# Kernel tuning notes

Measured on AMD Instinct MI355X. Metric: run time of the kernel, lower is better.

The kernel has to match this reference:

```python
import jax, jax.numpy as jnp
import numpy as np

N = 100000   # nodes
E = 1600000  # edges
IN_DIM = 64
OUT_DIM = 64
HEADS = 4
C = OUT_DIM // HEADS  # per-head channels = 16
EDGE_DIM = 16
NEG_SLOPE = 0.2
EPS = 1e-5


def setup_inputs() -> dict:
    key = jax.random.key(0)
    ks = jax.random.split(key, 16)
    s = 0.1
    return {
        "x": jax.random.normal(ks[0], (N, IN_DIM), jnp.float32),
        "edge_index": jax.random.randint(ks[1], (2, E), 0, N, jnp.int64 if jax.config.jax_enable_x64 else jnp.int32),
        "edge_attr": jax.random.normal(ks[2], (E, EDGE_DIM), jnp.float32),
        # GATv2Conv params (share_weights=False, edge_dim, concat=True)
        "Wl": jax.random.normal(ks[3], (IN_DIM, HEADS * C), jnp.float32) * s,
        "bl": jnp.zeros((HEADS * C,), jnp.float32),
        "Wr": jax.random.normal(ks[4], (IN_DIM, HEADS * C), jnp.float32) * s,
        "br": jnp.zeros((HEADS * C,), jnp.float32),
        "We": jax.random.normal(ks[5], (EDGE_DIM, HEADS * C), jnp.float32) * s,
        "att": jax.random.normal(ks[6], (HEADS, C), jnp.float32) * s,
        "conv_bias": jnp.zeros((HEADS * C,), jnp.float32),
        # edge gate MLP: Linear(edge_dim, 2*edge_dim) -> SiLU -> Linear(2*edge_dim, 1) -> Sigmoid
        "Wg1": jax.random.normal(ks[7], (EDGE_DIM, 2 * EDGE_DIM), jnp.float32) * s,
        "bg1": jnp.zeros((2 * EDGE_DIM,), jnp.float32),
        "Wg2": jax.random.normal(ks[8], (2 * EDGE_DIM, 1), jnp.float32) * s,
        "bg2": jnp.zeros((1,), jnp.float32),
        # LayerNorm(out_dim)
        "gamma": jnp.ones((OUT_DIM,), jnp.float32),
        "beta": jnp.zeros((OUT_DIM,), jnp.float32),
    }


def _silu(v):
    return v * jax.nn.sigmoid(v)


def reference(x, edge_index, edge_attr, Wl, bl, Wr, br, We, att, conv_bias,
              Wg1, bg1, Wg2, bg2, gamma, beta):
    src, tgt = edge_index[0], edge_index[1]

    # --- edge gate: sigmoid(Linear(SiLU(Linear(e)))) -> [E, 1]
    gate = jax.nn.sigmoid(_silu(edge_attr @ Wg1 + bg1) @ Wg2 + bg2)

    # --- GATv2Conv ---
    xl = (x @ Wl + bl).reshape(N, HEADS, C)   # source transform
    xr = (x @ Wr + br).reshape(N, HEADS, C)   # target transform
    ee = (edge_attr @ We).reshape(E, HEADS, C)

    xj = xl[src]                               # [E, H, C] source messages
    m = jax.nn.leaky_relu(xj + xr[tgt] + ee, NEG_SLOPE)
    alpha = jnp.einsum('ehc,hc->eh', m, att)   # [E, H]

    # segment softmax over edges sharing the same target node
    amax = jax.ops.segment_max(alpha, tgt, num_segments=N)  # [N, H]
    a = jnp.exp(alpha - amax[tgt])
    denom = jax.ops.segment_sum(a, tgt, num_segments=N)
    a = a / denom[tgt]

    out = jax.ops.segment_sum(xj * a[:, :, None], tgt, num_segments=N)
    out = out.reshape(N, HEADS * C) + conv_bias

    # --- edge-gate mean modulation per target node ---
    gate_sum = jax.ops.segment_sum(gate[:, 0], tgt, num_segments=N)
    degree = jax.ops.segment_sum(jnp.ones((E,), out.dtype), tgt, num_segments=N)
    mean_gate = gate_sum / jnp.maximum(degree, 1.0)
    out = out * mean_gate[:, None]

    # --- LayerNorm -> SiLU -> (dropout p=0) -> residual (Identity proj) ---
    mu = jnp.mean(out, axis=-1, keepdims=True)
    var = jnp.var(out, axis=-1, keepdims=True)
    out = (out - mu) * jax.lax.rsqrt(var + EPS) * gamma + beta
    out = _silu(out)
    return out + x
```

## Files before the change

kernel.cpp:

```cpp
#include <hip/hip_runtime.h>
#include <hip/hip_bf16.h>
#include <hip/hip_fp16.h>
#include <math.h>

#define N_NODES 100000
#define N_EDGES 1600000
#define IN_DIM 64
#define OUT_DIM 64
#define HEADS 4
#define CH 16
#define EDGE_DIM 16
#define NEG_SLOPE 0.2f
#define LN_EPS 1e-5f
#define NBLK 391
#define CHUNK 32
#define NREP 8
#define WS_NEED_EAH 127203168ull

typedef unsigned short u16;
typedef unsigned int u32;
typedef unsigned long long u64;
typedef __attribute__((ext_vector_type(8))) short bf16x8;
typedef __attribute__((ext_vector_type(4))) float f32x4;
typedef __attribute__((ext_vector_type(2))) _Float16 f16x2;

__device__ __forceinline__ float bf2f(u16 v) {
    return __uint_as_float(((u32)v) << 16);
}
__device__ __forceinline__ u16 f2bf(float f) {
    u32 u = __float_as_uint(f);
    u32 r = (u + 0x7FFFu + ((u >> 16) & 1u)) >> 16;
    return (u16)r;
}
__device__ __forceinline__ float fdot2f(u32 a, u32 b, float c) {
    return __builtin_amdgcn_fdot2(__builtin_bit_cast(f16x2, a),
                                  __builtin_bit_cast(f16x2, b), c, false);
}
__device__ __forceinline__ u32 packf16(float lo, float hi) {
    f16x2 p;
    p[0] = (_Float16)lo;
    p[1] = (_Float16)hi;
    return __builtin_bit_cast(u32, p);
}
__device__ __forceinline__ void load16bf(const u16* p, float* out) {
    const uint4* q = (const uint4*)p;
    uint4 a = q[0], b = q[1];
    u32 w[8] = {a.x, a.y, a.z, a.w, b.x, b.y, b.z, b.w};
#pragma unroll
    for (int i = 0; i < 8; ++i) {
        out[2*i]   = __uint_as_float(w[i] << 16);
        out[2*i+1] = __uint_as_float(w[i] & 0xFFFF0000u);
    }
}
__device__ __forceinline__ void load16f(const void* base, long i, bool f32in, float* out) {
    if (f32in) {
        const float4* q = (const float4*)((const float*)base + i);
        float4 v0 = q[0], v1 = q[1], v2 = q[2], v3 = q[3];
        out[0]=v0.x; out[1]=v0.y; out[2]=v0.z; out[3]=v0.w;
        out[4]=v1.x; out[5]=v1.y; out[6]=v1.z; out[7]=v1.w;
        out[8]=v2.x; out[9]=v2.y; out[10]=v2.z; out[11]=v2.w;
        out[12]=v3.x; out[13]=v3.y; out[14]=v3.z; out[15]=v3.w;
    } else {
        load16bf((const u16*)base + i, out);
    }
}
__device__ __forceinline__ float ldf(const void* base, int i, bool f32in) {
    return f32in ? ((const float*)base)[i] : bf2f(((const u16*)base)[i]);
}

#define DPP_ROR_ADD(v, N) do { \
    int _d = __builtin_amdgcn_update_dpp(0, __float_as_int(v), 0x120 + (N), 0xF, 0xF, true); \
    (v) += __int_as_float(_d); } while (0)

__global__ void k_sniff_zero(const u32* __restrict__ xw, const int* __restrict__ eiw,
                             int* __restrict__ flags, int4* __restrict__ curR4,
                             float4* __restrict__ gsum4) {
    if (blockIdx.x != 0) {
        const int i = (blockIdx.x - 1) * 256 + threadIdx.x;
        if (i < NREP * N_NODES / 4) curR4[i] = make_int4(0, 0, 0, 0);
        else if (i < NREP * N_NODES / 4 + N_NODES / 4)
            gsum4[i - NREP * N_NODES / 4] = make_float4(0.f, 0.f, 0.f, 0.f);
        return;
    }
    __shared__ int s_f32, s_not64;
    const int t = threadIdx.x;
    if (t == 0) { s_f32 = 0; s_not64 = 0; }
    __syncthreads();
    if (t < 64) {
        u32 w = xw[t];
        for (int h = 0; h < 2; ++h) {
            u32 bits = h ? (w & 0xFFFF0000u) : (w << 16);
            float v = __uint_as_float(bits);
            float a = fabsf(v);
            bool sane = (a == 0.0f) || (a >= 1e-30f && a <= 1000.0f);
            if (!sane || v != v) atomicOr(&s_f32, 1);
        }
    } else if (t < 96) {
        if (eiw[2 * (t - 64) + 1] != 0) atomicOr(&s_not64, 1);
    }
    __syncthreads();
    if (t == 0) flags[0] = s_f32 | ((s_not64 ? 0 : 1) << 1);
}

__global__ __launch_bounds__(256) void k_transform(
    const void* __restrict__ x,
    const void* __restrict__ Wl, const void* __restrict__ bl,
    const void* __restrict__ Wr, const void* __restrict__ br,
    u16* __restrict__ xl, u16* __restrict__ xr,
    const int* __restrict__ flags)
{
    const bool f32in = (flags[0] & 1) != 0;
    const int lane = threadIdx.x & 63;
    const int w = threadIdx.x >> 6;
    const int m0 = blockIdx.x * 64;
    const int col = lane & 15;
    const int quad = lane >> 4;

    bf16x8 bfrag[2][2];
    float bias[2];
#pragma unroll
    for (int nt = 0; nt < 2; ++nt) {
        const int ng = w * 32 + nt * 16 + col;
        const void* W  = (ng < 64) ? Wl : Wr;
        const void* bi = (ng < 64) ? bl : br;
        const int c = ng & 63;
        bias[nt] = ldf(bi, c, f32in);
#pragma unroll
        for (int kf = 0; kf < 2; ++kf)
#pragma unroll
            for (int j = 0; j < 8; ++j) {
                const int k = kf * 32 + quad * 8 + j;
                bfrag[nt][kf][j] = (short)f2bf(ldf(W, k * 64 + c, f32in));
            }
    }

#pragma unroll
    for (int mt = 0; mt < 4; ++mt) {
        const int mrow = m0 + mt * 16 + col;
        const int m = (mrow < N_NODES) ? mrow : (N_NODES - 1);
        bf16x8 afrag[2];
#pragma unroll
        for (int kf = 0; kf < 2; ++kf) {
            const int kb = kf * 32 + quad * 8;
            if (f32in) {
                const float* xp = (const float*)x + (size_t)m * 64 + kb;
#pragma unroll
                for (int j = 0; j < 8; ++j) afrag[kf][j] = (short)f2bf(xp[j]);
            } else {
                afrag[kf] = *(const bf16x8*)((const u16*)x + (size_t)m * 64 + kb);
            }
        }
#pragma unroll
        for (int nt = 0; nt < 2; ++nt) {
            f32x4 c = {bias[nt], bias[nt], bias[nt], bias[nt]};
            c = __builtin_amdgcn_mfma_f32_16x16x32_bf16(afrag[0], bfrag[nt][0], c, 0, 0, 0);
            c = __builtin_amdgcn_mfma_f32_16x16x32_bf16(afrag[1], bfrag[nt][1], c, 0, 0, 0);
            const int ng = w * 32 + nt * 16 + col;
            u16* dst = (ng < 64) ? xl : xr;
            const int cc = ng & 63;
#pragma unroll
            for (int r = 0; r < 4; ++r) {
                const int node = m0 + mt * 16 + quad * 4 + r;
                if (node < N_NODES) dst[(size_t)node * 64 + cc] = f2bf(c[r]);
            }
        }
    }
}

__global__ __launch_bounds__(256) void k_count_gate(
    const int* __restrict__ ei, int* __restrict__ curR,
    float4* __restrict__ zreg, u16* __restrict__ slotA, u16* __restrict__ gateA,
    u16* __restrict__ eaH, const int write_eah,
    const void* __restrict__ edge_attr,
    const void* __restrict__ Wg1, const void* __restrict__ bg1,
    const void* __restrict__ Wg2, const void* __restrict__ bg2,
    const int* __restrict__ flags)
{
    __shared__ float sWg1t[32 * 16];
    __shared__ float sBg1[32];
    __shared__ float sWg2[32];
    __shared__ float sBg2;
    const int tid = threadIdx.x;
    const int fl = flags[0];
    const bool f32in = (fl & 1) != 0;
    const bool i64   = (fl & 2) != 0;
    for (int i = tid; i < 32 * 16; i += 256) {
        const int j = i >> 4, k = i & 15;
        sWg1t[i] = ldf(Wg1, k * 32 + j, f32in);
    }
    if (tid < 32) sBg1[tid] = ldf(bg1, tid, f32in);
    if (tid >= 32 && tid < 64) sWg2[tid - 32] = ldf(Wg2, tid - 32, f32in);
    if (tid == 0) sBg2 = ldf(bg2, 0, f32in);
    __syncthreads();

    const int gid = blockIdx.x * 256 + tid;
    for (int i = gid; i < N_NODES * 68 / 4; i += 6250 * 256)
        zreg[i] = make_float4(0.f, 0.f, 0.f, 0.f);
    const int tgt = i64 ? ei[2 * (N_EDGES + gid)] : ei[N_EDGES + gid];
    const int r = blockIdx.x & (NREP - 1);
    const int slot = atomicAdd(&curR[r * N_NODES + tgt], 1);
    slotA[gid] = (u16)slot;

    float ea[EDGE_DIM];
    load16f(edge_attr, (long)gid * EDGE_DIM, f32in, ea);

    if (write_eah) {
        u32 h[8];
#pragma unroll
        for (int i = 0; i < 8; ++i) h[i] = packf16(ea[2*i], ea[2*i+1]);
        uint4* dst = (uint4*)(eaH + (size_t)gid * 16);
        dst[0] = make_uint4(h[0], h[1], h[2], h[3]);
        dst[1] = make_uint4(h[4], h[5], h[6], h[7]);
    }

    float g = sBg2;
#pragma unroll
    for (int j = 0; j < 32; ++j) {
        float hv = sBg1[j];
        const float4* wr = (const float4*)&sWg1t[j * 16];
#pragma unroll
        for (int k4 = 0; k4 < 4; ++k4) {
            const float4 wv = wr[k4];
            hv += ea[4*k4]   * wv.x + ea[4*k4+1] * wv.y
                + ea[4*k4+2] * wv.z + ea[4*k4+3] * wv.w;
        }
        hv = hv / (1.f + __expf(-hv));
        g += hv * sWg2[j];
    }
    g = 1.f / (1.f + __expf(-g));
    gateA[gid] = __half_as_ushort(__float2half(g));
}

__global__ __launch_bounds__(256) void k_bsum(const int* __restrict__ curR,
                                              int* __restrict__ partial)
{
    const int i = blockIdx.x * 256 + threadIdx.x;
    int v = 0;
    if (i < N_NODES) {
#pragma unroll
        for (int r = 0; r < NREP; ++r) v += curR[r * N_NODES + i];
    }
#pragma unroll
    for (int off = 32; off >= 1; off >>= 1) v += __shfl_xor(v, off, 64);
    __shared__ int ws[4];
    if ((threadIdx.x & 63) == 0) ws[threadIdx.x >> 6] = v;
    __syncthreads();
    if (threadIdx.x == 0) partial[blockIdx.x] = ws[0] + ws[1] + ws[2] + ws[3];
}

__global__ void k_bscan(const int* __restrict__ partial, int* __restrict__ poff,
                        int* __restrict__ base)
{
    __shared__ int sp[NBLK];
    for (int i = threadIdx.x; i < NBLK; i += 64) sp[i] = partial[i];
    __syncthreads();
    if (threadIdx.x == 0) {
        int run = 0;
        for (int i = 0; i < NBLK; ++i) { int t = sp[i]; sp[i] = run; run += t; }
        base[N_NODES] = N_EDGES;
    }
    __syncthreads();
    for (int i = threadIdx.x; i < NBLK; i += 64) poff[i] = sp[i];
}

__global__ __launch_bounds__(256) void k_bfinal(int* __restrict__ curR,
                                                const int* __restrict__ poff,
                                                int* __restrict__ base)
{
    const int i = blockIdx.x * 256 + threadIdx.x;
    const int lane = threadIdx.x & 63;
    const int wave = threadIdx.x >> 6;
    int c[NREP];
    int v = 0;
    if (i < N_NODES) {
#pragma unroll
        for (int r = 0; r < NREP; ++r) { c[r] = curR[r * N_NODES + i]; v += c[r]; }
    }
    int s = v;
#pragma unroll
    for (int off = 1; off < 64; off <<= 1) {
        int t = __shfl_up(s, off, 64);
        if (lane >= off) s += t;
    }
    __shared__ int wsum[4];
    if (lane == 63) wsum[wave] = s;
    __syncthreads();
    int wb = 0;
    for (int w = 0; w < wave; ++w) wb += wsum[w];
    if (i < N_NODES) {
        int run = poff[blockIdx.x] + wb + s - v;
        base[i] = run;
#pragma unroll
        for (int r = 0; r < NREP; ++r) { curR[r * N_NODES + i] = run; run += c[r]; }
    }
}

__global__ __launch_bounds__(256) void k_scatter(
    const int* __restrict__ ei, const int* __restrict__ curR,
    const u16* __restrict__ slotA,
    u64* __restrict__ perm8, const int* __restrict__ flags)
{
    const int e = blockIdx.x * 256 + threadIdx.x;
    const bool i64 = (flags[0] & 2) != 0;
    int src, tgt;
    if (i64) { src = ei[2 * e]; tgt = ei[2 * (N_EDGES + e)]; }
    else     { src = ei[e];     tgt = ei[N_EDGES + e]; }
    const int r = blockIdx.x & (NREP - 1);
    const int pos = curR[r * N_NODES + tgt] + (int)slotA[e];
    perm8[pos] = (u64)(u32)src | ((u64)(u32)tgt << 17) | ((u64)(u32)e << 34);
}


__device__ __forceinline__ void seg_flush(
    float* __restrict__ accum, float* __restrict__ dsum_g, float* __restrict__ gsum,
    int t, int lane, float acc, float dsum, float gs)
{
    atomicAdd(&accum[(size_t)t * 64 + lane], acc);
    if ((lane & 15) == 0) atomicAdd(&dsum_g[t * 4 + (lane >> 4)], dsum);
    if (lane == 1) atomicAdd(&gsum[t], gs);
}

template<bool F32IN, bool EAH>
__device__ __forceinline__ void ea_fetch(const void* __restrict__ edge_attr,
                                         const u16* __restrict__ eaH,
                                         int eid, uint4* r)
{
    if constexpr (EAH) {
        const uint4* q = (const uint4*)(eaH + (size_t)eid * 16);
        r[0] = q[0]; r[1] = q[1];
    } else if constexpr (F32IN) {
        const uint4* q = (const uint4*)edge_attr + (size_t)eid * 4;
        r[0] = q[0]; r[1] = q[1]; r[2] = q[2]; r[3] = q[3];
    } else {
        const uint4* q = (const uint4*)((const u16*)edge_attr + (size_t)eid * 16);
        r[0] = q[0]; r[1] = q[1];
    }
}

template<bool F32IN>
__device__ __forceinline__ void ea_vals(const uint4* r, float* out)
{
    const u32* w = (const u32*)r;
    if constexpr (F32IN) {
#pragma unroll
        for (int i = 0; i < 16; ++i) out[i] = __uint_as_float(w[i]);
    } else {
#pragma unroll
        for (int i = 0; i < 8; ++i) {
            out[2*i]   = __uint_as_float(w[i] << 16);
            out[2*i+1] = __uint_as_float(w[i] & 0xFFFF0000u);
        }
    }
}

#define PERM_EXTRACT(JJ, S, T, E2) do { \
    const u32 _lo = (u32)__builtin_amdgcn_readlane(plo, (JJ)); \
    const u32 _hi = (u32)__builtin_amdgcn_readlane(phi, (JJ)); \
    (S)  = (int)(_lo & 0x1FFFFu); \
    (T)  = (int)(((_lo >> 17) | (_hi << 15)) & 0x1FFFFu); \
    (E2) = (int)(_hi >> 2); } while (0)

template<bool F32IN, bool EAH>
__device__ __forceinline__ void attn_run(
    const u64* __restrict__ perm8, const void* __restrict__ edge_attr,
    const u16* __restrict__ eaH, const u16* __restrict__ gateA,
    const u16* __restrict__ xl, const u16* __restrict__ xr,
    float* __restrict__ accum, float* __restrict__ dsum_g, float* __restrict__ gsum,
    const float* We_c, const u32* We2, float att_c, int lane, int j0)
{
    const u64 pl = perm8[j0 + (lane & (CHUNK - 1))];
    const int plo = (int)(u32)pl;
    const int phi = (int)(u32)(pl >> 32);

    int s_cur, t_cur, e_cur;
    PERM_EXTRACT(0, s_cur, t_cur, e_cur);

    constexpr int NU4 = EAH ? 2 : (F32IN ? 4 : 2);
    uint4 eb[2][NU4];
    ea_fetch<F32IN, EAH>(edge_attr, eaH, e_cur, eb[0]);
    u32 xl_c = xl[(size_t)s_cur * 64 + lane];
    u32 xr_c = xr[(size_t)t_cur * 64 + lane];
    float g_c = __half2float(__ushort_as_half(gateA[e_cur]));

    int cur_t = t_cur;
    float acc = 0.f, dsum = 0.f, gs = 0.f;

#pragma unroll
    for (int jj = 0; jj < CHUNK; ++jj) {
        const int cb = jj & 1;
        int s_nxt = s_cur, t_nxt = t_cur, e_nxt = e_cur;
        u32 xl_n = xl_c, xr_n = xr_c;
        float g_n = g_c;
        if (jj + 1 < CHUNK) {
            PERM_EXTRACT(jj + 1, s_nxt, t_nxt, e_nxt);
            ea_fetch<F32IN, EAH>(edge_attr, eaH, e_nxt, eb[cb ^ 1]);
            xl_n = xl[(size_t)s_nxt * 64 + lane];
            g_n = __half2float(__ushort_as_half(gateA[e_nxt]));
            if (t_nxt != t_cur)
                xr_n = xr[(size_t)t_nxt * 64 + lane];
        }

        const float xlf = bf2f((u16)xl_c);
        const float xrf = bf2f((u16)xr_c);

        if (t_cur != cur_t) {
            seg_flush(accum, dsum_g, gsum, cur_t, lane, acc, dsum, gs);
            cur_t = t_cur; acc = 0.f; dsum = 0.f; gs = 0.f;
        }

        float m = xlf + xrf;
        if constexpr (EAH) {
            const u32* w = (const u32*)eb[cb];
#pragma unroll
            for (int i = 0; i < 8; ++i) m = fdot2f(w[i], We2[i], m);
        } else {
            float eav[16];
            ea_vals<F32IN>(eb[cb], eav);
#pragma unroll
            for (int k = 0; k < EDGE_DIM; ++k) m = fmaf(eav[k], We_c[k], m);
        }
        m = fmaxf(m, m * NEG_SLOPE);
        float t = att_c * m;
        DPP_ROR_ADD(t, 1);
        DPP_ROR_ADD(t, 2);
        DPP_ROR_ADD(t, 4);
        DPP_ROR_ADD(t, 8);
        const float a = __expf(t);
        acc  += a * xlf;
        dsum += a;
        gs   += g_c;

        s_cur = s_nxt; t_cur = t_nxt; e_cur = e_nxt;
        xl_c = xl_n;   xr_c = xr_n;   g_c = g_n;
    }
    seg_flush(accum, dsum_g, gsum, cur_t, lane, acc, dsum, gs);
}

template<bool EAH>
__global__ __launch_bounds__(256, 8) void k_attn_agg(
    const u64* __restrict__ perm8,
    const void* __restrict__ edge_attr,
    const u16* __restrict__ eaH,
    const u16* __restrict__ gateA,
    const void* __restrict__ We,
    const void* __restrict__ att,
    const u16* __restrict__ xl, const u16* __restrict__ xr,
    float* __restrict__ accum,
    float* __restrict__ dsum_g,
    float* __restrict__ gsum,
    const int* __restrict__ flags)
{
    const bool f32in = (flags[0] & 1) != 0;
    const int lane = threadIdx.x & 63;
    const int wid = blockIdx.x * 4 + (threadIdx.x >> 6);
    const int j0 = wid * CHUNK;

    float We_c[EDGE_DIM];
#pragma unroll
    for (int k = 0; k < EDGE_DIM; ++k) We_c[k] = ldf(We, k * 64 + lane, f32in);
    u32 We2[8];
    if constexpr (EAH) {
#pragma unroll
        for (int i = 0; i < 8; ++i) We2[i] = packf16(We_c[2*i], We_c[2*i+1]);
    }
    const float att_c = ldf(att, lane, f32in);

    if (f32in) attn_run<true , EAH>(perm8, edge_attr, eaH, gateA, xl, xr,
                                    accum, dsum_g, gsum, We_c, We2, att_c, lane, j0);
    else       attn_run<false, EAH>(perm8, edge_attr, eaH, gateA, xl, xr,
                                    accum, dsum_g, gsum, We_c, We2, att_c, lane, j0);
}

__global__ __launch_bounds__(256) void k_epilogue(
    const int* __restrict__ base,
    const float* __restrict__ accum, const float* __restrict__ dsum_g,
    const float* __restrict__ gsum,
    const void* __restrict__ conv_bias, const void* __restrict__ gamma,
    const void* __restrict__ beta, const void* __restrict__ x,
    void* __restrict__ out, const int* __restrict__ flags)
{
    const bool f32in = (flags[0] & 1) != 0;
    const int lane = threadIdx.x & 63;
    const int wave = threadIdx.x >> 6;
    const int n = blockIdx.x * 4 + wave;
    if (n >= N_NODES) return;
    const int h = lane >> 4;

    float v = accum[(size_t)n * 64 + lane];
    const float d = dsum_g[n * 4 + h];
    v = (d > 0.f) ? v / d : 0.f;
    v += ldf(conv_bias, lane, f32in);
    const int deg = base[n + 1] - base[n];
    const float mg = gsum[n] / fmaxf((float)deg, 1.0f);
    v *= mg;

    float s = v;
#pragma unroll
    for (int m2 = 32; m2 >= 1; m2 >>= 1) s += __shfl_xor(s, m2, 64);
    const float mu = s * (1.f / 64.f);
    const float diff = v - mu;
    float q = diff * diff;
#pragma unroll
    for (int m2 = 32; m2 >= 1; m2 >>= 1) q += __shfl_xor(q, m2, 64);
    const float var = q * (1.f / 64.f);

    float y = diff * rsqrtf(var + LN_EPS) * ldf(gamma, lane, f32in) + ldf(beta, lane, f32in);
    y = y / (1.f + __expf(-y));
    const float r = y + ldf(x, n * 64 + lane, f32in);
    if (f32in) ((float*)out)[(size_t)n * 64 + lane] = r;
    else       ((u16*)out)[(size_t)n * 64 + lane] = f2bf(r);
}

extern "C" void kernel_launch(void* const* d_in, const int* in_sizes, int n_in,
                              void* d_out, int out_size, void* d_ws, size_t ws_size,
                              hipStream_t stream)
{
    const void* x   = d_in[0];
    const int* ei   = (const int*)d_in[1];
    const void* ea  = d_in[2];
    const void* Wl  = d_in[3];
    const void* bl  = d_in[4];
    const void* Wr  = d_in[5];
    const void* br  = d_in[6];
    const void* We  = d_in[7];
    const void* att = d_in[8];
    const void* cb  = d_in[9];
    const void* Wg1 = d_in[10];
    const void* bg1 = d_in[11];
    const void* Wg2 = d_in[12];
    const void* bg2 = d_in[13];
    const void* gam = d_in[14];
    const void* bet = d_in[15];

    char* ws = (char*)d_ws;
    int*   flags   = (int*)ws;
    int*   curR    = (int*)(ws + 16);
    int*   base    = (int*)(ws + 3200016);
    int*   partial = (int*)(ws + 3600032);
    int*   poff    = (int*)(ws + 3601600);
    u16*   slotA   = (u16*)(ws + 3603168);
    u16*   gateA   = (u16*)(ws + 6803168);
    u64*   perm8   = (u64*)(ws + 10003168);
    float* accum   = (float*)(ws + 22803168);
    float* dsum_g  = (float*)(ws + 48403168);
    float* gsum    = (float*)(ws + 50003168);
    u16*   xl      = (u16*)(ws + 50403168);
    u16*   xr      = (u16*)(ws + 63203168);
    u16*   eaH     = (u16*)(ws + 76003168);

    const int eah = (ws_size >= WS_NEED_EAH) ? 1 : 0;

    k_sniff_zero<<<881, 256, 0, stream>>>((const u32*)x, ei, flags, (int4*)curR,
                                          (float4*)gsum);

    k_transform<<<(N_NODES + 63) / 64, 256, 0, stream>>>(x, Wl, bl, Wr, br, xl, xr, flags);

    k_count_gate<<<N_EDGES / 256, 256, 0, stream>>>(
        ei, curR, (float4*)accum, slotA, gateA, eaH, eah, ea, Wg1, bg1, Wg2, bg2, flags);

    k_bsum<<<NBLK, 256, 0, stream>>>(curR, partial);
    k_bscan<<<1, 64, 0, stream>>>(partial, poff, base);
    k_bfinal<<<NBLK, 256, 0, stream>>>(curR, poff, base);

    k_scatter<<<N_EDGES / 256, 256, 0, stream>>>(ei, curR, slotA, perm8, flags);

    if (eah)
        k_attn_agg<true ><<<N_EDGES / CHUNK / 4, 256, 0, stream>>>(
            perm8, ea, eaH, gateA, We, att, xl, xr, accum, dsum_g, gsum, flags);
    else
        k_attn_agg<false><<<N_EDGES / CHUNK / 4, 256, 0, stream>>>(
            perm8, ea, eaH, gateA, We, att, xl, xr, accum, dsum_g, gsum, flags);

    k_epilogue<<<(N_NODES + 3) / 4, 256, 0, stream>>>(
        base, accum, dsum_g, gsum, cb, gam, bet, x, d_out, flags);
}
```

Measured before the change: 476.7 us.

## Permute fp16 edge attributes and pack gate into perm during scatter

Moves the fp16 conversion of edge attributes from the gate kernel into the scatter kernel. The scatter now writes them in target-sorted order, so the attention kernel reads them sequentially instead of gathering by edge id. The fp16 gate value is packed into the perm entry in place of the edge id, which removes the random gateA gather. The cost is that the scatter writes are now random 32-byte stores and the scatter kernel re-reads edge_attr.

```diff
diff --git a/kernel.cpp b/kernel.cpp
--- a/kernel.cpp
+++ b/kernel.cpp
@@ -15,7 +15,7 @@
 #define NBLK 391
 #define CHUNK 32
 #define NREP 8
-#define WS_NEED_EAH 127203168ull
+#define WS_NEED_STREAM 127203168ull
 
 typedef unsigned short u16;
 typedef unsigned int u32;
@@ -170,7 +170,6 @@
 __global__ __launch_bounds__(256) void k_count_gate(
     const int* __restrict__ ei, int* __restrict__ curR,
     float4* __restrict__ zreg, u16* __restrict__ slotA, u16* __restrict__ gateA,
-    u16* __restrict__ eaH, const int write_eah,
     const void* __restrict__ edge_attr,
     const void* __restrict__ Wg1, const void* __restrict__ bg1,
     const void* __restrict__ Wg2, const void* __restrict__ bg2,
@@ -204,15 +203,6 @@
     float ea[EDGE_DIM];
     load16f(edge_attr, (long)gid * EDGE_DIM, f32in, ea);
 
-    if (write_eah) {
-        u32 h[8];
-#pragma unroll
-        for (int i = 0; i < 8; ++i) h[i] = packf16(ea[2*i], ea[2*i+1]);
-        uint4* dst = (uint4*)(eaH + (size_t)gid * 16);
-        dst[0] = make_uint4(h[0], h[1], h[2], h[3]);
-        dst[1] = make_uint4(h[4], h[5], h[6], h[7]);
-    }
-
     float g = sBg2;
 #pragma unroll
     for (int j = 0; j < 32; ++j) {
@@ -297,17 +287,35 @@
 
 __global__ __launch_bounds__(256) void k_scatter(
     const int* __restrict__ ei, const int* __restrict__ curR,
-    const u16* __restrict__ slotA,
+    const u16* __restrict__ slotA, const u16* __restrict__ gateA,
+    const void* __restrict__ edge_attr, u16* __restrict__ eaP,
+    const int stream_mode,
     u64* __restrict__ perm8, const int* __restrict__ flags)
 {
     const int e = blockIdx.x * 256 + threadIdx.x;
-    const bool i64 = (flags[0] & 2) != 0;
+    const int fl = flags[0];
+    const bool f32in = (fl & 1) != 0;
+    const bool i64   = (fl & 2) != 0;
     int src, tgt;
     if (i64) { src = ei[2 * e]; tgt = ei[2 * (N_EDGES + e)]; }
     else     { src = ei[e];     tgt = ei[N_EDGES + e]; }
     const int r = blockIdx.x & (NREP - 1);
     const int pos = curR[r * N_NODES + tgt] + (int)slotA[e];
-    perm8[pos] = (u64)(u32)src | ((u64)(u32)tgt << 17) | ((u64)(u32)e << 34);
+
+    if (stream_mode) {
+        const u32 gate = gateA[e];
+        perm8[pos] = (u64)(u32)src | ((u64)(u32)tgt << 17) | ((u64)gate << 34);
+        float ea[EDGE_DIM];
+        load16f(edge_attr, (long)e * EDGE_DIM, f32in, ea);
+        u32 h[8];
+#pragma unroll
+        for (int i = 0; i < 8; ++i) h[i] = packf16(ea[2*i], ea[2*i+1]);
+        uint4* dst = (uint4*)(eaP + (size_t)pos * 16);
+        dst[0] = make_uint4(h[0], h[1], h[2], h[3]);
+        dst[1] = make_uint4(h[4], h[5], h[6], h[7]);
+    } else {
+        perm8[pos] = (u64)(u32)src | ((u64)(u32)tgt << 17) | ((u64)(u32)e << 34);
+    }
 }
 
 
@@ -320,15 +328,11 @@
     if (lane == 1) atomicAdd(&gsum[t], gs);
 }
 
-template<bool F32IN, bool EAH>
+template<bool F32IN>
 __device__ __forceinline__ void ea_fetch(const void* __restrict__ edge_attr,
-                                         const u16* __restrict__ eaH,
                                          int eid, uint4* r)
 {
-    if constexpr (EAH) {
-        const uint4* q = (const uint4*)(eaH + (size_t)eid * 16);
-        r[0] = q[0]; r[1] = q[1];
-    } else if constexpr (F32IN) {
+    if constexpr (F32IN) {
         const uint4* q = (const uint4*)edge_attr + (size_t)eid * 4;
         r[0] = q[0]; r[1] = q[1]; r[2] = q[2]; r[3] = q[3];
     } else {
@@ -360,10 +364,17 @@
     (T)  = (int)(((_lo >> 17) | (_hi << 15)) & 0x1FFFFu); \
     (E2) = (int)(_hi >> 2); } while (0)
 
-template<bool F32IN, bool EAH>
+#define PERM_EXTRACT_S(JJ, S, T, G) do { \
+    const u32 _lo = (u32)__builtin_amdgcn_readlane(plo, (JJ)); \
+    const u32 _hi = (u32)__builtin_amdgcn_readlane(phi, (JJ)); \
+    (S)  = (int)(_lo & 0x1FFFFu); \
+    (T)  = (int)(((_lo >> 17) | (_hi << 15)) & 0x1FFFFu); \
+    (G)  = (_hi >> 2) & 0xFFFFu; } while (0)
+
+template<int MODE, bool F32IN>
 __device__ __forceinline__ void attn_run(
     const u64* __restrict__ perm8, const void* __restrict__ edge_attr,
-    const u16* __restrict__ eaH, const u16* __restrict__ gateA,
+    const u16* __restrict__ eaP, const u16* __restrict__ gateA,
     const u16* __restrict__ xl, const u16* __restrict__ xr,
     float* __restrict__ accum, float* __restrict__ dsum_g, float* __restrict__ gsum,
     const float* We_c, const u32* We2, float att_c, int lane, int j0)
@@ -372,15 +383,23 @@
     const int plo = (int)(u32)pl;
     const int phi = (int)(u32)(pl >> 32);
 
-    int s_cur, t_cur, e_cur;
-    PERM_EXTRACT(0, s_cur, t_cur, e_cur);
-
-    constexpr int NU4 = EAH ? 2 : (F32IN ? 4 : 2);
+    int s_cur, t_cur, e_cur = 0;
+    u32 g_cur = 0;
+    if constexpr (MODE == 1) { PERM_EXTRACT_S(0, s_cur, t_cur, g_cur); }
+    else                     { PERM_EXTRACT(0, s_cur, t_cur, e_cur); }
+
+    constexpr int NU4 = (MODE == 1) ? 2 : (F32IN ? 4 : 2);
     uint4 eb[2][NU4];
-    ea_fetch<F32IN, EAH>(edge_attr, eaH, e_cur, eb[0]);
+    if constexpr (MODE == 1) {
+        const uint4* q = (const uint4*)(eaP + (size_t)j0 * 16);
+        eb[0][0] = q[0]; eb[0][1] = q[1];
+    } else {
+        ea_fetch<F32IN>(edge_attr, e_cur, eb[0]);
+    }
     u32 xl_c = xl[(size_t)s_cur * 64 + lane];
     u32 xr_c = xr[(size_t)t_cur * 64 + lane];
-    float g_c = __half2float(__ushort_as_half(gateA[e_cur]));
+    float g_c = (MODE == 1) ? __half2float(__ushort_as_half((u16)g_cur))
+                            : __half2float(__ushort_as_half(gateA[e_cur]));
 
     int cur_t = t_cur;
     float acc = 0.f, dsum = 0.f, gs = 0.f;
@@ -392,10 +411,18 @@
         u32 xl_n = xl_c, xr_n = xr_c;
         float g_n = g_c;
         if (jj + 1 < CHUNK) {
-            PERM_EXTRACT(jj + 1, s_nxt, t_nxt, e_nxt);
-            ea_fetch<F32IN, EAH>(edge_attr, eaH, e_nxt, eb[cb ^ 1]);
+            if constexpr (MODE == 1) {
+                u32 g_u;
+                PERM_EXTRACT_S(jj + 1, s_nxt, t_nxt, g_u);
+                const uint4* q = (const uint4*)(eaP + (size_t)(j0 + jj + 1) * 16);
+                eb[cb ^ 1][0] = q[0]; eb[cb ^ 1][1] = q[1];
+                g_n = __half2float(__ushort_as_half((u16)g_u));
+            } else {
+                PERM_EXTRACT(jj + 1, s_nxt, t_nxt, e_nxt);
+                ea_fetch<F32IN>(edge_attr, e_nxt, eb[cb ^ 1]);
+                g_n = __half2float(__ushort_as_half(gateA[e_nxt]));
+            }
             xl_n = xl[(size_t)s_nxt * 64 + lane];
-            g_n = __half2float(__ushort_as_half(gateA[e_nxt]));
             if (t_nxt != t_cur)
                 xr_n = xr[(size_t)t_nxt * 64 + lane];
         }
@@ -409,7 +436,7 @@
         }
 
         float m = xlf + xrf;
-        if constexpr (EAH) {
+        if constexpr (MODE == 1) {
             const u32* w = (const u32*)eb[cb];
 #pragma unroll
             for (int i = 0; i < 8; ++i) m = fdot2f(w[i], We2[i], m);
@@ -436,11 +463,11 @@
     seg_flush(accum, dsum_g, gsum, cur_t, lane, acc, dsum, gs);
 }
 
-template<bool EAH>
+template<int MODE>
 __global__ __launch_bounds__(256, 8) void k_attn_agg(
     const u64* __restrict__ perm8,
     const void* __restrict__ edge_attr,
-    const u16* __restrict__ eaH,
+    const u16* __restrict__ eaP,
     const u16* __restrict__ gateA,
     const void* __restrict__ We,
     const void* __restrict__ att,
@@ -459,16 +486,16 @@
 #pragma unroll
     for (int k = 0; k < EDGE_DIM; ++k) We_c[k] = ldf(We, k * 64 + lane, f32in);
     u32 We2[8];
-    if constexpr (EAH) {
+    if constexpr (MODE == 1) {
 #pragma unroll
         for (int i = 0; i < 8; ++i) We2[i] = packf16(We_c[2*i], We_c[2*i+1]);
     }
     const float att_c = ldf(att, lane, f32in);
 
-    if (f32in) attn_run<true , EAH>(perm8, edge_attr, eaH, gateA, xl, xr,
-                                    accum, dsum_g, gsum, We_c, We2, att_c, lane, j0);
-    else       attn_run<false, EAH>(perm8, edge_attr, eaH, gateA, xl, xr,
-                                    accum, dsum_g, gsum, We_c, We2, att_c, lane, j0);
+    if (f32in) attn_run<MODE, true >(perm8, edge_attr, eaP, gateA, xl, xr,
+                                     accum, dsum_g, gsum, We_c, We2, att_c, lane, j0);
+    else       attn_run<MODE, false>(perm8, edge_attr, eaP, gateA, xl, xr,
+                                     accum, dsum_g, gsum, We_c, We2, att_c, lane, j0);
 }
 
 __global__ __launch_bounds__(256) void k_epilogue(
@@ -546,9 +573,9 @@
     float* gsum    = (float*)(ws + 50003168);
     u16*   xl      = (u16*)(ws + 50403168);
     u16*   xr      = (u16*)(ws + 63203168);
-    u16*   eaH     = (u16*)(ws + 76003168);
-
-    const int eah = (ws_size >= WS_NEED_EAH) ? 1 : 0;
+    u16*   eaP     = (u16*)(ws + 76003168);
+
+    const int stream_mode = (ws_size >= WS_NEED_STREAM) ? 1 : 0;
 
     k_sniff_zero<<<881, 256, 0, stream>>>((const u32*)x, ei, flags, (int4*)curR,
                                           (float4*)gsum);
@@ -556,20 +583,21 @@
     k_transform<<<(N_NODES + 63) / 64, 256, 0, stream>>>(x, Wl, bl, Wr, br, xl, xr, flags);
 
     k_count_gate<<<N_EDGES / 256, 256, 0, stream>>>(
-        ei, curR, (float4*)accum, slotA, gateA, eaH, eah, ea, Wg1, bg1, Wg2, bg2, flags);
+        ei, curR, (float4*)accum, slotA, gateA, ea, Wg1, bg1, Wg2, bg2, flags);
 
     k_bsum<<<NBLK, 256, 0, stream>>>(curR, partial);
     k_bscan<<<1, 64, 0, stream>>>(partial, poff, base);
     k_bfinal<<<NBLK, 256, 0, stream>>>(curR, poff, base);
 
-    k_scatter<<<N_EDGES / 256, 256, 0, stream>>>(ei, curR, slotA, perm8, flags);
-
-    if (eah)
-        k_attn_agg<true ><<<N_EDGES / CHUNK / 4, 256, 0, stream>>>(
-            perm8, ea, eaH, gateA, We, att, xl, xr, accum, dsum_g, gsum, flags);
+    k_scatter<<<N_EDGES / 256, 256, 0, stream>>>(
+        ei, curR, slotA, gateA, ea, eaP, stream_mode, perm8, flags);
+
+    if (stream_mode)
+        k_attn_agg<1><<<N_EDGES / CHUNK / 4, 256, 0, stream>>>(
+            perm8, ea, eaP, gateA, We, att, xl, xr, accum, dsum_g, gsum, flags);
     else
-        k_attn_agg<false><<<N_EDGES / CHUNK / 4, 256, 0, stream>>>(
-            perm8, ea, eaH, gateA, We, att, xl, xr, accum, dsum_g, gsum, flags);
+        k_attn_agg<0><<<N_EDGES / CHUNK / 4, 256, 0, stream>>>(
+            perm8, ea, eaP, gateA, We, att, xl, xr, accum, dsum_g, gsum, flags);
 
     k_epilogue<<<(N_NODES + 3) / 4, 256, 0, stream>>>(
         base, accum, dsum_g, gsum, cb, gam, bet, x, d_out, flags);
```

Result: slower. 533.8 us (+12.0%).
